# Performance work log

Hardware: AMD Instinct MI355X
Metric: run time of the kernel (lower is better)

The kernel has to match this reference:

```python
import jax, jax.numpy as jnp
import numpy as np

B, S = 32, 512          # batch, blocks-per-graph
E = 512                 # embedding_size
BLOCK, EDGE = 4, 1
EWM = BLOCK * BLOCK * (EDGE + 1)   # 32, edge_with_mask_block_size
IN = 2 * E              # nn input size (1024)
HID = 2048              # decoder hidden layer
OUT = 4 * E + EWM       # 2080
K = 10                  # kernel_count
RATE = 0.005


def setup_inputs() -> dict:
    key = jax.random.key(0)
    ks = jax.random.split(key, 12)
    s = 0.02
    return {
        "embedding_l": jax.random.normal(ks[0], (B, S, E), jnp.float32),
        "embedding_r": jax.random.normal(ks[1], (B, S, E), jnp.float32),
        # main decoder MLP: IN -> HID -> OUT
        "nn_w1": jax.random.normal(ks[2], (IN, HID), jnp.float32) * s,
        "nn_b1": jnp.zeros((HID,), jnp.float32),
        "nn_w2": jax.random.normal(ks[3], (HID, OUT), jnp.float32) * s,
        "nn_b2": jnp.zeros((OUT,), jnp.float32),
        # 10 expert kernels stacked: IN -> IN -> IN+1 (dropout inactive at inference)
        "ker_w1": jax.random.normal(ks[4], (K, IN, IN), jnp.float32) * s,
        "ker_b1": jnp.zeros((K, IN), jnp.float32),
        "ker_w2": jax.random.normal(ks[5], (K, IN, IN + 1), jnp.float32) * s,
        "ker_b2": jnp.zeros((K, IN + 1), jnp.float32),
    }


def reference(embedding_l, embedding_r, nn_w1, nn_b1, nn_w2, nn_b2,
              ker_w1, ker_b1, ker_w2, ker_b2):
    # [B, S, 2E]
    prev = jnp.concatenate([embedding_l, embedding_r], axis=-1)

    # main decoder MLP
    h = jax.nn.relu(prev @ nn_w1 + nn_b1)
    out = h @ nn_w2 + nn_b2

    decoded = out[..., :EWM]
    dbl = out[..., EWM:EWM + 2 * E]
    ratio = out[..., EWM + 2 * E:]

    decoded = decoded.reshape(B, S, BLOCK, BLOCK, EDGE + 1)

    # weighted_average(new, old, ratio): sigmoid-gated blend
    g = jax.nn.sigmoid(ratio)
    dbl = dbl * g + prev * (1.0 - g)

    # 10 expert kernels, vectorized over kernel axis k
    kh = jax.nn.relu(jnp.einsum('bsd,kdh->bksh', dbl, ker_w1) + ker_b1[None, :, None, :])
    kr = jnp.einsum('bksh,kho->bkso', kh, ker_w2) + ker_b2[None, :, None, :]  # [B,K,S,2E+1]

    attn = jax.nn.sigmoid(kr[..., -1:])            # [B,K,S,1]
    changes_raw = kr[..., :-1]                      # [B,K,S,2E]
    attn = attn / jnp.sum(attn, axis=2, keepdims=True)

    # matmul(changes^T, attn) == attention-weighted sum over S
    changes = jnp.sum(changes_raw * attn, axis=2)   # [B,K,2E]
    agg = jnp.mean(changes, axis=1)                 # [B,2E]

    dbl = dbl * (1.0 - RATE) + agg[:, None, :] * RATE

    new_l = dbl[..., :E]
    new_r = dbl[..., E:]
    return (decoded, new_l, new_r)
```

## Files before the change

### kernel.cpp

```cpp
#include <hip/hip_runtime.h>
#include <math.h>


typedef __bf16 bf16x8 __attribute__((ext_vector_type(8)));
typedef float  f32x4  __attribute__((ext_vector_type(4)));

__device__ __forceinline__ float bf2f(unsigned short u) {
  unsigned int x = ((unsigned int)u) << 16;
  return __builtin_bit_cast(float, x);
}
__device__ __forceinline__ unsigned short f2bf(float f) {
  unsigned int x = __builtin_bit_cast(unsigned int, f);
  x += 0x7fffu + ((x >> 16) & 1u);
  return (unsigned short)(x >> 16);
}
__device__ __forceinline__ void gload_lds16(const void* g, void* l) {
  __builtin_amdgcn_global_load_lds(
      (const __attribute__((address_space(1))) unsigned int*)g,
      (__attribute__((address_space(3))) unsigned int*)l, 16, 0, 0);
}

#define OFF_XB    0ull
#define OFF_W1T   (OFF_XB  + 33554432ull)
#define OFF_HB    (OFF_W1T + 4194304ull)
#define OFF_W2T   (OFF_HB  + 67108864ull)
#define OFF_OUT   (OFF_W2T + 8912896ull)
#define OFF_KW1T  OFF_OUT
#define OFF_KH    (OFF_KW1T + 20971520ull)
#define OFF_WPART (OFF_KH   + 33554432ull)
#define OFF_SIG   (OFF_WPART+ 1048576ull)
#define OFF_DEN   (OFF_SIG  + 65536ull)
#define OFF_TPART (OFF_DEN  + 1024ull)
#define OFF_AGG   (OFF_TPART+ 1048576ull)
#define OFF_VBUF  (OFF_AGG  + 131072ull)


__global__ void convert_X(const float* __restrict__ el, const float* __restrict__ er,
                          unsigned short* __restrict__ Xb) {
  long gid = (long)blockIdx.x * blockDim.x + threadIdx.x;
  long e = gid * 4;
  long r = e >> 10; int c = (int)(e & 1023);
  const float* s = (c < 512) ? (el + r * 512 + c) : (er + r * 512 + (c - 512));
  float4 v = *(const float4*)s;
  ushort4 o; o.x = f2bf(v.x); o.y = f2bf(v.y); o.z = f2bf(v.z); o.w = f2bf(v.w);
  *(ushort4*)(Xb + e) = o;
}

__global__ void transpose_cvt(const float* __restrict__ src, unsigned short* __restrict__ dst,
                              int R, int C) {
  __shared__ float tile[32][33];
  long zoff = (long)blockIdx.z * R * C;
  src += zoff; dst += zoff;
  int tx = threadIdx.x, ty = threadIdx.y;
  long r0 = (long)blockIdx.y * 32, c0 = (long)blockIdx.x * 32;
#pragma unroll
  for (int j = 0; j < 32; j += 8)
    tile[ty + j][tx] = src[(r0 + ty + j) * C + c0 + tx];
  __syncthreads();
#pragma unroll
  for (int j = 0; j < 32; j += 8)
    dst[(c0 + ty + j) * R + r0 + tx] = f2bf(tile[tx][ty + j]);
}

template <int RELU, int WB, int GV>
__global__ __launch_bounds__(256) void gemm128(
    const unsigned short* __restrict__ A, const unsigned short* __restrict__ Bt,
    const float* __restrict__ bias, unsigned short* __restrict__ Cb,
    float* __restrict__ Cf, const float* __restrict__ gvec,
    float* __restrict__ gout, int K, int Nvalid, int ldc) {
  __shared__ unsigned short As[128 * 32];
  __shared__ unsigned short Bs[128 * 32];
  const int tid = threadIdx.x;
  const int wv = tid >> 6, ln = tid & 63;
  const long m0 = (long)blockIdx.x * 128;
  const long n0 = (long)blockIdx.y * 128;
  const int wm = wv >> 1, wn = wv & 1;
  f32x4 acc[4][4] = {};
  for (int kt = 0; kt < K; kt += 32) {
#pragma unroll
    for (int i = 0; i < 2; ++i) {
      int c = tid + i * 256;
      int r = c >> 2, kp = (c & 3) * 8;
      gload_lds16(A + (m0 + r) * K + kt + kp, (void*)&As[(i * 256 + wv * 64) * 8]);
      gload_lds16(Bt + (n0 + r) * K + kt + kp, (void*)&Bs[(i * 256 + wv * 64) * 8]);
    }
    __syncthreads();
    bf16x8 af[4], bfr[4];
#pragma unroll
    for (int mi = 0; mi < 4; ++mi)
      af[mi] = *(const bf16x8*)&As[((wm * 64 + mi * 16 + (ln & 15)) * 4 + (ln >> 4)) * 8];
#pragma unroll
    for (int ni = 0; ni < 4; ++ni)
      bfr[ni] = *(const bf16x8*)&Bs[((wn * 64 + ni * 16 + (ln & 15)) * 4 + (ln >> 4)) * 8];
#pragma unroll
    for (int mi = 0; mi < 4; ++mi)
#pragma unroll
      for (int ni = 0; ni < 4; ++ni)
        acc[mi][ni] = __builtin_amdgcn_mfma_f32_16x16x32_bf16(af[mi], bfr[ni], acc[mi][ni], 0, 0, 0);
    __syncthreads();
  }
  const int lr = ln >> 4, lc = ln & 15;
  long colv[4]; bool okv[4]; float bv[4], gvv[4];
#pragma unroll
  for (int ni = 0; ni < 4; ++ni) {
    colv[ni] = n0 + wn * 64 + ni * 16 + lc;
    okv[ni] = colv[ni] < Nvalid;
    bv[ni] = okv[ni] ? bias[colv[ni]] : 0.f;
    gvv[ni] = GV ? gvec[colv[ni]] : 0.f;
  }
#pragma unroll
  for (int mi = 0; mi < 4; ++mi) {
#pragma unroll
    for (int j = 0; j < 4; ++j) {
      long row = m0 + wm * 64 + mi * 16 + lr * 4 + j;
      float p = 0.f;
#pragma unroll
      for (int ni = 0; ni < 4; ++ni) {
        float v = acc[mi][ni][j] + bv[ni];
        if (RELU) v = fmaxf(v, 0.f);
        if (okv[ni]) {
          if (WB) Cb[row * ldc + colv[ni]] = f2bf(v);
          else    Cf[row * ldc + colv[ni]] = v;
        }
        if (GV) p += v * gvv[ni];
      }
      if (GV) {
#pragma unroll
        for (int off = 1; off < 16; off <<= 1) p += __shfl_xor(p, off);
        if (lc == 0) gout[(blockIdx.y * 2 + wn) * 16384 + row] = p;
      }
    }
  }
}

__global__ void postproc(const float* __restrict__ OUT, const float* __restrict__ el,
                         const float* __restrict__ er, float* __restrict__ dec,
                         float* __restrict__ dblf, unsigned short* __restrict__ dblb) {
  long r = blockIdx.x;
  int t = threadIdx.x;
  const float* orow = OUT + r * 2080;
  if (t < 8) {
    float4 v = *(const float4*)(orow + t * 4);
    *(float4*)(dec + r * 32 + t * 4) = v;
  }
  int c = t * 4;
  float4 d  = *(const float4*)(orow + 32 + c);
  float4 rt = *(const float4*)(orow + 1056 + c);
  const float* pp = (c < 512) ? (el + r * 512 + c) : (er + r * 512 + (c - 512));
  float4 p = *(const float4*)pp;
  float4 o; float g;
  g = 1.f / (1.f + expf(-rt.x)); o.x = d.x * g + p.x * (1.f - g);
  g = 1.f / (1.f + expf(-rt.y)); o.y = d.y * g + p.y * (1.f - g);
  g = 1.f / (1.f + expf(-rt.z)); o.z = d.z * g + p.z * (1.f - g);
  g = 1.f / (1.f + expf(-rt.w)); o.w = d.w * g + p.w * (1.f - g);
  *(float4*)(dblf + r * 1024 + c) = o;
  ushort4 ob; ob.x = f2bf(o.x); ob.y = f2bf(o.y); ob.z = f2bf(o.z); ob.w = f2bf(o.w);
  *(ushort4*)(dblb + r * 1024 + c) = ob;
}

__global__ void extract_v(const float* __restrict__ kw2, float* __restrict__ vbuf) {
  int i = blockIdx.x * 256 + threadIdx.x;
  int k = i >> 10, h = i & 1023;
  vbuf[i] = kw2[(long)k * 1024 * 1025 + (long)h * 1025 + 1024];
}

__global__ __launch_bounds__(512) void sigma_den(const float* __restrict__ wpart,
                                                 const float* __restrict__ kb2k,
                                                 float* __restrict__ sig, float* __restrict__ den) {
  int b = blockIdx.x, t = threadIdx.x;
  int row = b * 512 + t;
  float x = kb2k[1024];
#pragma unroll
  for (int c = 0; c < 16; ++c) x += wpart[c * 16384 + row];
  float s = 1.f / (1.f + expf(-x));
  sig[row] = s;
  float v = s;
#pragma unroll
  for (int off = 32; off >= 1; off >>= 1) v += __shfl_down(v, off);
  __shared__ float ps[8];
  if ((t & 63) == 0) ps[t >> 6] = v;
  __syncthreads();
  if (t == 0) { float dsum = 0.f; for (int i = 0; i < 8; ++i) dsum += ps[i]; den[b] = dsum; }
}

__global__ __launch_bounds__(256) void t_reduce(const unsigned short* __restrict__ KH,
                                                const float* __restrict__ sig,
                                                float* __restrict__ tpart) {
  int b = blockIdx.x, hb = blockIdx.y, sc = blockIdx.z;
  int h = hb * 256 + threadIdx.x;
  __shared__ float sl[64];
  if (threadIdx.x < 64) sl[threadIdx.x] = sig[b * 512 + sc * 64 + threadIdx.x];
  __syncthreads();
  float acc = 0.f;
  const unsigned short* base = KH + ((long)b * 512 + sc * 64) * 1024 + h;
#pragma unroll 8
  for (int s = 0; s < 64; ++s) acc += sl[s] * bf2f(base[(long)s * 1024]);
  tpart[sc * 32768 + b * 1024 + h] = acc;
}

__global__ __launch_bounds__(256) void small_gemm(const float* __restrict__ tpart,
                                                  const float* __restrict__ kw2k,
                                                  const float* __restrict__ kb2k,
                                                  const float* __restrict__ den,
                                                  float* __restrict__ aggsum) {
  int b = blockIdx.x, ob = blockIdx.y, hc = blockIdx.z;
  int o = ob * 256 + threadIdx.x;
  __shared__ float tl[256];
  float tv = 0.f;
#pragma unroll
  for (int sc = 0; sc < 8; ++sc) tv += tpart[sc * 32768 + b * 1024 + hc * 256 + threadIdx.x];
  tl[threadIdx.x] = tv;
  __syncthreads();
  float acc = 0.f;
#pragma unroll 4
  for (int h = 0; h < 256; ++h) acc += tl[h] * kw2k[(long)(hc * 256 + h) * 1025 + o];
  float dn = den[b];
  if (hc == 0) acc += kb2k[o] * dn;
  atomicAdd(&aggsum[b * 1024 + o], acc / dn);
}

__global__ void final_out(const float* __restrict__ dblf, const float* __restrict__ agg,
                          float* __restrict__ out) {
  long gid = (long)blockIdx.x * 256 + threadIdx.x;
  long e = gid * 4;
  long r = e >> 10; int c = (int)(e & 1023);
  int b = (int)(r >> 9);
  float4 d = *(const float4*)(dblf + e);
  float4 a = *(const float4*)(agg + b * 1024 + c);
  float4 o;
  o.x = d.x * 0.995f + a.x * 0.0005f;
  o.y = d.y * 0.995f + a.y * 0.0005f;
  o.z = d.z * 0.995f + a.z * 0.0005f;
  o.w = d.w * 0.995f + a.w * 0.0005f;
  float* dst = (c < 512) ? (out + 524288 + r * 512 + c)
                         : (out + 524288 + 8388608 + r * 512 + (c - 512));
  *(float4*)dst = o;
}

extern "C" void kernel_launch(void* const* d_in, const int* in_sizes, int n_in,
                              void* d_out, int out_size, void* d_ws, size_t ws_size,
                              hipStream_t stream) {
  const float* el  = (const float*)d_in[0];
  const float* er  = (const float*)d_in[1];
  const float* w1  = (const float*)d_in[2];
  const float* b1  = (const float*)d_in[3];
  const float* w2  = (const float*)d_in[4];
  const float* b2  = (const float*)d_in[5];
  const float* kw1 = (const float*)d_in[6];
  const float* kb1 = (const float*)d_in[7];
  const float* kw2 = (const float*)d_in[8];
  const float* kb2 = (const float*)d_in[9];
  float* out = (float*)d_out;
  char* ws = (char*)d_ws;

  unsigned short* Xb   = (unsigned short*)(ws + OFF_XB);
  unsigned short* W1t  = (unsigned short*)(ws + OFF_W1T);
  unsigned short* Hb   = (unsigned short*)(ws + OFF_HB);
  unsigned short* W2t  = (unsigned short*)(ws + OFF_W2T);
  float*          OUTf = (float*)(ws + OFF_OUT);
  unsigned short* dblb = (unsigned short*)(ws + OFF_XB);
  float*          dblf = (float*)(ws + OFF_HB);
  unsigned short* KW1t = (unsigned short*)(ws + OFF_KW1T);
  unsigned short* KHb  = (unsigned short*)(ws + OFF_KH);
  float* wpart = (float*)(ws + OFF_WPART);
  float* sig   = (float*)(ws + OFF_SIG);
  float* den   = (float*)(ws + OFF_DEN);
  float* tpart = (float*)(ws + OFF_TPART);
  float* agg   = (float*)(ws + OFF_AGG);
  float* vbuf  = (float*)(ws + OFF_VBUF);

  convert_X<<<16384, 256, 0, stream>>>(el, er, Xb);
  transpose_cvt<<<dim3(64, 32, 1), dim3(32, 8), 0, stream>>>(w1, W1t, 1024, 2048);
  transpose_cvt<<<dim3(65, 64, 1), dim3(32, 8), 0, stream>>>(w2, W2t, 2048, 2080);

  gemm128<1, 1, 0><<<dim3(128, 16, 1), 256, 0, stream>>>(
      Xb, W1t, b1, Hb, nullptr, nullptr, nullptr, 1024, 2048, 2048);
  gemm128<0, 0, 0><<<dim3(128, 17, 1), 256, 0, stream>>>(
      Hb, W2t, b2, nullptr, OUTf, nullptr, nullptr, 2048, 2080, 2080);

  postproc<<<16384, 256, 0, stream>>>(OUTf, el, er, out, dblf, dblb);

  transpose_cvt<<<dim3(32, 32, 10), dim3(32, 8), 0, stream>>>(kw1, KW1t, 1024, 1024);
  extract_v<<<40, 256, 0, stream>>>(kw2, vbuf);
  hipMemsetAsync(agg, 0, 32 * 1024 * 4, stream);

  for (int k = 0; k < 10; ++k) {
    const float* kw2k = kw2 + (long)k * 1024 * 1025;
    const float* kb2k = kb2 + (long)k * 1025;
    gemm128<1, 1, 1><<<dim3(128, 8, 1), 256, 0, stream>>>(
        dblb, KW1t + (long)k * 1024 * 1024, kb1 + k * 1024, KHb, nullptr,
        vbuf + k * 1024, wpart, 1024, 1024, 1024);
    sigma_den<<<32, 512, 0, stream>>>(wpart, kb2k, sig, den);
    t_reduce<<<dim3(32, 4, 8), 256, 0, stream>>>(KHb, sig, tpart);
    small_gemm<<<dim3(32, 4, 4), 256, 0, stream>>>(tpart, kw2k, kb2k, den, agg);
  }

  final_out<<<16384, 256, 0, stream>>>(dblf, agg, out);
}
```

Measured before the change: 1.623 ms.

## Replace 128x128 GEMM with 256x256 tile, 4-stage async LDS pipeline

Replaces the single-buffered 128x128 bf16 MFMA GEMM with a 256x256 tile kernel that uses 512 threads. It stages K-slices through a 4-deep LDS ring with global_load_lds and explicit vmcnt waits, so loads overlap compute. It also adds an XOR swizzle on the LDS layout to avoid bank conflicts, workgroup index swizzling for L2 locality, and s_setprio around the MFMA block. The 128KB LDS footprint limits occupancy to one block per CU. Partial N tiles are handled by clamping B rows to a padded bound.

```diff
diff --git a/kernel.cpp b/kernel.cpp
--- a/kernel.cpp
+++ b/kernel.cpp
@@ -19,6 +19,8 @@
       (const __attribute__((address_space(1))) unsigned int*)g,
       (__attribute__((address_space(3))) unsigned int*)l, 16, 0, 0);
 }
+#define WAITV(n) asm volatile("s_waitcnt vmcnt(" #n ")" ::: "memory")
+#define MEMFENCE() asm volatile("" ::: "memory")
 
 #define OFF_XB    0ull
 #define OFF_W1T   (OFF_XB  + 33554432ull)
@@ -63,56 +65,97 @@
 }
 
 template <int RELU, int WB, int GV>
-__global__ __launch_bounds__(256) void gemm128(
+__global__ __launch_bounds__(512, 2) void gemm256(
     const unsigned short* __restrict__ A, const unsigned short* __restrict__ Bt,
     const float* __restrict__ bias, unsigned short* __restrict__ Cb,
     float* __restrict__ Cf, const float* __restrict__ gvec,
-    float* __restrict__ gout, int K, int Nvalid, int ldc) {
-  __shared__ unsigned short As[128 * 32];
-  __shared__ unsigned short Bs[128 * 32];
+    float* __restrict__ gout, int K, int NB, int Nvalid, int ldc, int nbt) {
+  __shared__ unsigned short lds[65536];
   const int tid = threadIdx.x;
   const int wv = tid >> 6, ln = tid & 63;
-  const long m0 = (long)blockIdx.x * 128;
-  const long n0 = (long)blockIdx.y * 128;
-  const int wm = wv >> 1, wn = wv & 1;
-  f32x4 acc[4][4] = {};
-  for (int kt = 0; kt < K; kt += 32) {
+  const int nwg = gridDim.x;
+  const int swz = (blockIdx.x & 7) * (nwg >> 3) + (blockIdx.x >> 3);
+  const long m0 = (long)(swz / NB) * 256;
+  const long n0 = (long)(swz % NB) * 256;
+  const int wr = wv >> 2, wc = wv & 3;
+  const int lr = ln >> 4, lc = ln & 15;
+  const int nt = K >> 5;
+
+  f32x4 acc[8][4] = {};
+
+  auto stage = [&](int t) {
+    const int buf = t & 3;
+    const long kt = (long)t << 5;
+    unsigned short* la = &lds[buf * 16384];
+    unsigned short* lb = la + 8192;
 #pragma unroll
     for (int i = 0; i < 2; ++i) {
-      int c = tid + i * 256;
-      int r = c >> 2, kp = (c & 3) * 8;
-      gload_lds16(A + (m0 + r) * K + kt + kp, (void*)&As[(i * 256 + wv * 64) * 8]);
-      gload_lds16(Bt + (n0 + r) * K + kt + kp, (void*)&Bs[(i * 256 + wv * 64) * 8]);
-    }
-    __syncthreads();
-    bf16x8 af[4], bfr[4];
-#pragma unroll
-    for (int mi = 0; mi < 4; ++mi)
-      af[mi] = *(const bf16x8*)&As[((wm * 64 + mi * 16 + (ln & 15)) * 4 + (ln >> 4)) * 8];
-#pragma unroll
-    for (int ni = 0; ni < 4; ++ni)
-      bfr[ni] = *(const bf16x8*)&Bs[((wn * 64 + ni * 16 + (ln & 15)) * 4 + (ln >> 4)) * 8];
-#pragma unroll
-    for (int mi = 0; mi < 4; ++mi)
+      int c = tid + i * 512;
+      int row = c >> 2, cc = c & 3;
+      int sc = cc ^ (row & 3);
+      gload_lds16(A + (m0 + row) * K + kt + sc * 8, la + c * 8);
+    }
+#pragma unroll
+    for (int i = 0; i < 2; ++i) {
+      int c = tid + i * 512;
+      int row = c >> 2, cc = c & 3;
+      int sc = cc ^ (row & 3);
+      long brow = n0 + row;
+      if (brow >= nbt) brow = nbt - 1;
+      gload_lds16(Bt + brow * K + kt + sc * 8, lb + c * 8);
+    }
+  };
+
+  auto compute = [&](int t) {
+    const int buf = t & 3;
+    const unsigned short* la = &lds[buf * 16384];
+    const unsigned short* lb = la + 8192;
+    bf16x8 bfr[4];
+#pragma unroll
+    for (int ni = 0; ni < 4; ++ni) {
+      int row = wc * 64 + ni * 16 + lc;
+      bfr[ni] = *(const bf16x8*)&lb[row * 32 + ((lr ^ (row & 3)) * 8)];
+    }
+    __builtin_amdgcn_s_setprio(1);
+#pragma unroll
+    for (int mi = 0; mi < 8; ++mi) {
+      int row = wr * 128 + mi * 16 + lc;
+      bf16x8 af = *(const bf16x8*)&la[row * 32 + ((lr ^ (row & 3)) * 8)];
 #pragma unroll
       for (int ni = 0; ni < 4; ++ni)
-        acc[mi][ni] = __builtin_amdgcn_mfma_f32_16x16x32_bf16(af[mi], bfr[ni], acc[mi][ni], 0, 0, 0);
-    __syncthreads();
-  }
-  const int lr = ln >> 4, lc = ln & 15;
+        acc[mi][ni] = __builtin_amdgcn_mfma_f32_16x16x32_bf16(af, bfr[ni], acc[mi][ni], 0, 0, 0);
+    }
+    __builtin_amdgcn_s_setprio(0);
+  };
+
+  stage(0); stage(1); stage(2);
+  WAITV(8);
+  __builtin_amdgcn_s_barrier();
+  MEMFENCE();
+
+  for (int t = 0; t < nt; ++t) {
+    if (t + 3 < nt) stage(t + 3);
+    compute(t);
+    if (t + 3 < nt)      WAITV(8);
+    else if (t + 2 < nt) WAITV(4);
+    else                 WAITV(0);
+    __builtin_amdgcn_s_barrier();
+    MEMFENCE();
+  }
+
   long colv[4]; bool okv[4]; float bv[4], gvv[4];
 #pragma unroll
   for (int ni = 0; ni < 4; ++ni) {
-    colv[ni] = n0 + wn * 64 + ni * 16 + lc;
+    colv[ni] = n0 + wc * 64 + ni * 16 + lc;
     okv[ni] = colv[ni] < Nvalid;
     bv[ni] = okv[ni] ? bias[colv[ni]] : 0.f;
     gvv[ni] = GV ? gvec[colv[ni]] : 0.f;
   }
 #pragma unroll
-  for (int mi = 0; mi < 4; ++mi) {
+  for (int mi = 0; mi < 8; ++mi) {
 #pragma unroll
     for (int j = 0; j < 4; ++j) {
-      long row = m0 + wm * 64 + mi * 16 + lr * 4 + j;
+      long row = m0 + wr * 128 + mi * 16 + lr * 4 + j;
       float p = 0.f;
 #pragma unroll
       for (int ni = 0; ni < 4; ++ni) {
@@ -127,7 +170,7 @@
       if (GV) {
 #pragma unroll
         for (int off = 1; off < 16; off <<= 1) p += __shfl_xor(p, off);
-        if (lc == 0) gout[(blockIdx.y * 2 + wn) * 16384 + row] = p;
+        if (lc == 0) gout[((n0 >> 6) + wc) * 16384 + row] = p;
       }
     }
   }
@@ -273,10 +316,10 @@
   transpose_cvt<<<dim3(64, 32, 1), dim3(32, 8), 0, stream>>>(w1, W1t, 1024, 2048);
   transpose_cvt<<<dim3(65, 64, 1), dim3(32, 8), 0, stream>>>(w2, W2t, 2048, 2080);
 
-  gemm128<1, 1, 0><<<dim3(128, 16, 1), 256, 0, stream>>>(
-      Xb, W1t, b1, Hb, nullptr, nullptr, nullptr, 1024, 2048, 2048);
-  gemm128<0, 0, 0><<<dim3(128, 17, 1), 256, 0, stream>>>(
-      Hb, W2t, b2, nullptr, OUTf, nullptr, nullptr, 2048, 2080, 2080);
+  gemm256<1, 1, 0><<<512, 512, 0, stream>>>(
+      Xb, W1t, b1, Hb, nullptr, nullptr, nullptr, 1024, 8, 2048, 2048, 2048);
+  gemm256<0, 0, 0><<<576, 512, 0, stream>>>(
+      Hb, W2t, b2, nullptr, OUTf, nullptr, nullptr, 2048, 9, 2080, 2080, 2176);
 
   postproc<<<16384, 256, 0, stream>>>(OUTf, el, er, out, dblf, dblb);
 
@@ -287,9 +330,9 @@
   for (int k = 0; k < 10; ++k) {
     const float* kw2k = kw2 + (long)k * 1024 * 1025;
     const float* kb2k = kb2 + (long)k * 1025;
-    gemm128<1, 1, 1><<<dim3(128, 8, 1), 256, 0, stream>>>(
+    gemm256<1, 1, 1><<<256, 512, 0, stream>>>(
         dblb, KW1t + (long)k * 1024 * 1024, kb1 + k * 1024, KHb, nullptr,
-        vbuf + k * 1024, wpart, 1024, 1024, 1024);
+        vbuf + k * 1024, wpart, 1024, 4, 1024, 1024, 1024);
     sigma_den<<<32, 512, 0, stream>>>(wpart, kb2k, sig, den);
     t_reduce<<<dim3(32, 4, 8), 256, 0, stream>>>(KHb, sig, tpart);
     small_gemm<<<dim3(32, 4, 4), 256, 0, stream>>>(tpart, kw2k, kb2k, den, agg);
```

Result: faster. 1.415 ms (-12.8%).
